# Performance work log

Measured on AMD Instinct MI355X. Metric: run time of the kernel, lower is better.

The kernel has to match this reference:

```python
import jax, jax.numpy as jnp
import numpy as np
from jax.ops import segment_sum

N = 100000
E = 2500000
F = 2
H = 32
L = 2


def setup_inputs() -> dict:
    key = jax.random.key(0)
    ks = jax.random.split(key, 12)
    s = 0.1
    node_features = jax.random.normal(ks[0], (N, F), dtype=jnp.float32)
    edge_index = jax.random.randint(ks[1], (2, E), 0, N, dtype=jnp.int64)
    W_in = jax.random.normal(ks[2], (F, H), dtype=jnp.float32) * s
    b_in = jnp.zeros((H,), dtype=jnp.float32)
    W_upd = jax.random.normal(ks[3], (L, 2 * H, H), dtype=jnp.float32) * s
    b_upd = jnp.zeros((L, H), dtype=jnp.float32)
    We1 = jax.random.normal(ks[4], (2 * H, H), dtype=jnp.float32) * s
    be1 = jnp.zeros((H,), dtype=jnp.float32)
    We2 = jax.random.normal(ks[5], (H, 1), dtype=jnp.float32) * s
    be2 = jnp.zeros((1,), dtype=jnp.float32)
    return {"node_features": node_features, "edge_index": edge_index,
            "W_in": W_in, "b_in": b_in, "W_upd": W_upd, "b_upd": b_upd,
            "We1": We1, "be1": be1, "We2": We2, "be2": be2}


def reference(node_features, edge_index, W_in, b_in, W_upd, b_upd, We1, be1, We2, be2):
    row, col = edge_index[0], edge_index[1]
    h = jax.nn.relu(node_features @ W_in + b_in)  # [N, H]
    # degree of each row node (bincount, clamped to >=1)
    deg = segment_sum(jnp.ones((E,), dtype=jnp.float32), row, num_segments=N)
    deg = jnp.maximum(deg, 1.0)[:, None]  # [N, 1]
    for l in range(L):
        agg = segment_sum(h[col], row, num_segments=N) / deg  # gather + scatter-add + normalize
        h = jax.nn.relu(jnp.concatenate([h, agg], axis=-1) @ W_upd[l] + b_upd[l])
    edge_feat = jnp.concatenate([h[row], h[col]], axis=-1)  # [E, 2H]
    hidden = jax.nn.relu(edge_feat @ We1 + be1)
    flux = (hidden @ We2 + be2)[:, 0]  # [E]
    return flux
```

## Files before the change

kernel.cpp:

```cpp
#include <hip/hip_runtime.h>
#include <hip/hip_fp16.h>

#define NN 100000
#define NE 2500000
#define RANGE 256
#define NBUCK 391
#define CHUNK 16384
#define NBLK_A ((NE + CHUNK - 1) / CHUNK)
#define BCAP 8192

__device__ __forceinline__ float relu_(float x){ return fmaxf(x, 0.f); }


__global__ __launch_bounds__(512) void k_histA(const int* __restrict__ row,
                                               int* __restrict__ btot,
                                               int* __restrict__ blockhist)
{
  __shared__ int hist[NBUCK];
  int t = threadIdx.x;
  for (int i = t; i < NBUCK; i += 512) hist[i] = 0;
  __syncthreads();
  int e0 = blockIdx.x * CHUNK + t;
#pragma unroll
  for (int k = 0; k < CHUNK / 512; ++k) {
    int e = e0 + k * 512;
    if (e < NE) atomicAdd(&hist[row[e] >> 8], 1);
  }
  __syncthreads();
  for (int i = t; i < NBUCK; i += 512) {
    int c = hist[i];
    blockhist[(size_t)i * NBLK_A + blockIdx.x] = c;
    if (c) atomicAdd(&btot[i], c);
  }
}

__global__ __launch_bounds__(512) void k_scanA(const int* __restrict__ btot,
                                               int* __restrict__ bbase)
{
  __shared__ int s[512];
  int t = threadIdx.x;
  int my = (t < NBUCK) ? btot[t] : 0;
  s[t] = my;
  __syncthreads();
  for (int off = 1; off < 512; off <<= 1) {
    int v = (t >= off) ? s[t - off] : 0;
    __syncthreads();
    s[t] += v;
    __syncthreads();
  }
  if (t < NBUCK) bbase[t] = s[t] - my;
  if (t == 0) bbase[NBUCK] = NE;
}

__global__ __launch_bounds__(512) void k_colscan(int* __restrict__ blockhist,
                                                 const int* __restrict__ bbase)
{
  __shared__ int s[512];
  int i = blockIdx.x, t = threadIdx.x;
  int* rowp = blockhist + (size_t)i * NBLK_A;
  int my = (t < NBLK_A) ? rowp[t] : 0;
  s[t] = my;
  __syncthreads();
  for (int off = 1; off < 512; off <<= 1) {
    int v = (t >= off) ? s[t - off] : 0;
    __syncthreads();
    s[t] += v;
    __syncthreads();
  }
  if (t < NBLK_A) rowp[t] = bbase[i] + s[t] - my;
}

__global__ __launch_bounds__(512) void k_partition(
    const int* __restrict__ row, const int* __restrict__ col,
    const int* __restrict__ blockhist, unsigned int* __restrict__ keys)
{
  __shared__ int cur[NBUCK];
  __shared__ int base[NBUCK];
  int t = threadIdx.x, b = blockIdx.x;
  for (int i = t; i < NBUCK; i += 512) {
    base[i] = blockhist[(size_t)i * NBLK_A + b];
    cur[i] = 0;
  }
  __syncthreads();
  int e0 = b * CHUNK + t;
#pragma unroll
  for (int k = 0; k < CHUNK / 512; ++k) {
    int e = e0 + k * 512;
    if (e < NE) {
      int r = row[e];
      int bi = r >> 8;
      int idx = atomicAdd(&cur[bi], 1);
      keys[base[bi] + idx] = ((unsigned)col[e] << 8) | (unsigned)(r & 255);
    }
  }
}

__global__ __launch_bounds__(512) void k_passB_l1(
    const int* __restrict__ bbase, const unsigned int* __restrict__ keys,
    const float* __restrict__ nf, const float* __restrict__ Win,
    const float* __restrict__ bin, const float* __restrict__ W,
    const float* __restrict__ bupd,
    int* __restrict__ ecol, int* __restrict__ rowptr,
    __half* __restrict__ h16b)
{
  __shared__ unsigned keysl[BCAP];
  __shared__ int hist[RANGE];
  __shared__ int sc[RANGE];
  __shared__ int segs[RANGE];
  __shared__ int sege[RANGE];
  __shared__ float Ws[2048];
  __shared__ float bs[32];
  int t = threadIdx.x, b = blockIdx.x;
  for (int i = t; i < 2048; i += 512) Ws[i] = W[i];
  if (t < 32) bs[t] = bupd[t];
  int s0 = bbase[b], e0 = bbase[b + 1];
  int cnt = e0 - s0;
  if (t < RANGE) hist[t] = 0;
  __syncthreads();
  for (int i = t; i < cnt; i += 512) {
    unsigned k = keys[s0 + i];
    if (i < BCAP) keysl[i] = k;
    atomicAdd(&hist[k & 255u], 1);
  }
  __syncthreads();
  int my = (t < RANGE) ? hist[t] : 0;
  if (t < RANGE) sc[t] = my;
  __syncthreads();
  for (int off = 1; off < RANGE; off <<= 1) {
    int v = 0;
    if (t < RANGE && t >= off) v = sc[t - off];
    __syncthreads();
    if (t < RANGE) sc[t] += v;
    __syncthreads();
  }
  if (t < RANGE) {
    int ex = sc[t] - my;
    int n = b * RANGE + t;
    if (n <= NN) rowptr[n] = s0 + ex;
    segs[t] = ex;
    sege[t] = sc[t];
    hist[t] = ex;
  }
  __syncthreads();
  for (int i = t; i < cnt; i += 512) {
    unsigned key = (i < BCAP) ? keysl[i] : keys[s0 + i];
    int rl = (int)(key & 255u);
    int idx = atomicAdd(&hist[rl], 1);
    ecol[s0 + idx] = (int)(key >> 8);
  }
  __syncthreads();

  const float2* nf2 = (const float2*)nf;
  for (int slot = t; slot < RANGE * 4; slot += 512) {
    int node = slot >> 2, q = slot & 3;
    int n = b * RANGE + node;
    if (n >= NN) continue;
    float w0[8], w1[8], bb[8];
#pragma unroll
    for (int j = 0; j < 8; ++j) {
      w0[j] = Win[q * 8 + j];
      w1[j] = Win[32 + q * 8 + j];
      bb[j] = bin[q * 8 + j];
    }
    int ss = segs[node], ee = sege[node];
    float acc[8];
#pragma unroll
    for (int j = 0; j < 8; ++j) acc[j] = 0.f;
    int i = ss;
    for (; i + 2 <= ee; i += 2) {
      int c0 = ecol[s0 + i], c1 = ecol[s0 + i + 1];
      float2 f0 = nf2[c0];
      float2 f1 = nf2[c1];
#pragma unroll
      for (int j = 0; j < 8; ++j) {
        acc[j] += relu_(fmaf(f0.x, w0[j], fmaf(f0.y, w1[j], bb[j])));
        acc[j] += relu_(fmaf(f1.x, w0[j], fmaf(f1.y, w1[j], bb[j])));
      }
    }
    if (i < ee) {
      float2 f = nf2[ecol[s0 + i]];
#pragma unroll
      for (int j = 0; j < 8; ++j)
        acc[j] += relu_(fmaf(f.x, w0[j], fmaf(f.y, w1[j], bb[j])));
    }
    float dinv = 1.0f / fmaxf((float)(ee - ss), 1.0f);
    float g[8], a[8];
    float2 fn = nf2[n];
#pragma unroll
    for (int j = 0; j < 8; ++j) {
      g[j] = acc[j] * dinv;
      a[j] = relu_(fmaf(fn.x, w0[j], fmaf(fn.y, w1[j], bb[j])));
    }
    float o[8];
#pragma unroll
    for (int j = 0; j < 8; ++j) o[j] = bs[q * 8 + j];
#pragma unroll
    for (int src = 0; src < 4; ++src) {
#pragma unroll
      for (int k = 0; k < 8; ++k) {
        float xh = __shfl(a[k], src, 4);
        float xg = __shfl(g[k], src, 4);
        const float* wr1 = Ws + (src * 8 + k) * 32 + q * 8;
        const float* wr2 = Ws + (32 + src * 8 + k) * 32 + q * 8;
#pragma unroll
        for (int j = 0; j < 8; ++j) {
          o[j] = fmaf(xh, wr1[j], o[j]);
          o[j] = fmaf(xg, wr2[j], o[j]);
        }
      }
    }
    uint4 pk;
    __half2* pp = (__half2*)&pk;
#pragma unroll
    for (int k = 0; k < 4; ++k)
      pp[k] = __floats2half2_rn(relu_(o[2*k]), relu_(o[2*k+1]));
    ((uint4*)h16b)[(size_t)n * 4 + q] = pk;
  }
}

__global__ __launch_bounds__(256) void k_agg_update2_uv(
    const int* __restrict__ rowptr, const int* __restrict__ ecol,
    const __half* __restrict__ h16in, const float* __restrict__ W,
    const float* __restrict__ b, const float* __restrict__ We1,
    const float* __restrict__ be1, __half* __restrict__ u,
    __half* __restrict__ v)
{
  __shared__ float Ws[2048];
  __shared__ float Es[2048];
  __shared__ float bs[32];
  __shared__ float bes[32];
  __shared__ float xs[64][65];
  int t = threadIdx.x;
  for (int i = t; i < 2048; i += 256) { Ws[i] = W[i]; Es[i] = We1[i]; }
  if (t < 32) { bs[t] = b[t]; bes[t] = be1[t]; }
  int q = t & 3, ln = t >> 2;
  int n = blockIdx.x * 64 + ln;
  bool act = (n < NN);
  const uint4* hv = (const uint4*)h16in;

  float acc[8];
#pragma unroll
  for (int j = 0; j < 8; ++j) acc[j] = 0.f;
  if (act) {
    int s = rowptr[n], e = rowptr[n + 1];
    int i = s;
    for (; i + 2 <= e; i += 2) {
      int c0 = ecol[i], c1 = ecol[i + 1];
      uint4 x0 = hv[c0 * 4 + q];
      uint4 x1 = hv[c1 * 4 + q];
      const __half2* p0 = (const __half2*)&x0;
      const __half2* p1 = (const __half2*)&x1;
#pragma unroll
      for (int k = 0; k < 4; ++k) {
        float2 f0 = __half22float2(p0[k]);
        float2 f1 = __half22float2(p1[k]);
        acc[2*k]   += f0.x + f1.x;
        acc[2*k+1] += f0.y + f1.y;
      }
    }
    if (i < e) {
      uint4 x = hv[ecol[i] * 4 + q];
      const __half2* hp = (const __half2*)&x;
#pragma unroll
      for (int k = 0; k < 4; ++k) {
        float2 f = __half22float2(hp[k]);
        acc[2*k] += f.x; acc[2*k+1] += f.y;
      }
    }
    float dinv = 1.0f / fmaxf((float)(e - s), 1.0f);
    uint4 hx = hv[n * 4 + q];
    const __half2* hp = (const __half2*)&hx;
#pragma unroll
    for (int k = 0; k < 4; ++k) {
      float2 f = __half22float2(hp[k]);
      xs[ln][q*8 + 2*k]     = f.x;
      xs[ln][q*8 + 2*k + 1] = f.y;
      xs[ln][32 + q*8 + 2*k]     = acc[2*k] * dinv;
      xs[ln][32 + q*8 + 2*k + 1] = acc[2*k+1] * dinv;
    }
  }
  __syncthreads();
  float h2[8];
#pragma unroll
  for (int j = 0; j < 8; ++j) h2[j] = bs[q*8 + j];
  if (act) {
    for (int k = 0; k < 64; ++k) {
      float xk = xs[ln][k];
      const float* wr = Ws + k * 32 + q * 8;
#pragma unroll
      for (int j = 0; j < 8; ++j) h2[j] = fmaf(xk, wr[j], h2[j]);
    }
#pragma unroll
    for (int j = 0; j < 8; ++j) h2[j] = relu_(h2[j]);
  }
  __syncthreads();
  if (act) {
#pragma unroll
    for (int j = 0; j < 8; ++j) xs[ln][q*8 + j] = h2[j];
  }
  __syncthreads();
  if (!act) return;
  float au[8], av[8];
#pragma unroll
  for (int j = 0; j < 8; ++j) { au[j] = bes[q*8 + j]; av[j] = 0.f; }
  for (int k = 0; k < 32; ++k) {
    float hk = xs[ln][k];
    const float* wu = Es + k * 32 + q * 8;
    const float* wv = Es + (32 + k) * 32 + q * 8;
#pragma unroll
    for (int j = 0; j < 8; ++j) {
      au[j] = fmaf(hk, wu[j], au[j]);
      av[j] = fmaf(hk, wv[j], av[j]);
    }
  }
  uint4 pu, pv;
  __half2* up = (__half2*)&pu;
  __half2* vp = (__half2*)&pv;
#pragma unroll
  for (int k = 0; k < 4; ++k) {
    up[k] = __floats2half2_rn(au[2*k], au[2*k+1]);
    vp[k] = __floats2half2_rn(av[2*k], av[2*k+1]);
  }
  ((uint4*)u)[n * 4 + q] = pu;
  ((uint4*)v)[n * 4 + q] = pv;
}

__global__ __launch_bounds__(256) void k_flux(
    const int* __restrict__ row, const int* __restrict__ col,
    const __half* __restrict__ u, const __half* __restrict__ v,
    const float* __restrict__ We2, const float* __restrict__ be2,
    float* __restrict__ out)
{
  int gid = blockIdx.x * 256 + threadIdx.x;
  int e = gid >> 2, q = gid & 3;
  if (e >= NE) return;
  int r = row[e], c = col[e];
  uint4 ua = ((const uint4*)u)[r * 4 + q];
  uint4 vb = ((const uint4*)v)[c * 4 + q];
  const __half2* ah = (const __half2*)&ua;
  const __half2* bh = (const __half2*)&vb;
  const float4* w4 = (const float4*)(We2 + q * 8);
  float4 w0 = w4[0], w1 = w4[1];
  float p = 0.f;
  {
    float2 a = __half22float2(ah[0]), b = __half22float2(bh[0]);
    p += relu_(a.x + b.x) * w0.x + relu_(a.y + b.y) * w0.y;
    a = __half22float2(ah[1]); b = __half22float2(bh[1]);
    p += relu_(a.x + b.x) * w0.z + relu_(a.y + b.y) * w0.w;
    a = __half22float2(ah[2]); b = __half22float2(bh[2]);
    p += relu_(a.x + b.x) * w1.x + relu_(a.y + b.y) * w1.y;
    a = __half22float2(ah[3]); b = __half22float2(bh[3]);
    p += relu_(a.x + b.x) * w1.z + relu_(a.y + b.y) * w1.w;
  }
  p += __shfl_xor(p, 1, 4);
  p += __shfl_xor(p, 2, 4);
  if (q == 0) out[e] = p + be2[0];
}

extern "C" void kernel_launch(void* const* d_in, const int* in_sizes, int n_in,
                              void* d_out, int out_size, void* d_ws, size_t ws_size,
                              hipStream_t stream) {
  const float* nf   = (const float*)d_in[0];
  const int*   ei   = (const int*)d_in[1];
  const float* Win  = (const float*)d_in[2];
  const float* bin  = (const float*)d_in[3];
  const float* Wupd = (const float*)d_in[4];
  const float* bupd = (const float*)d_in[5];
  const float* We1  = (const float*)d_in[6];
  const float* be1  = (const float*)d_in[7];
  const float* We2  = (const float*)d_in[8];
  const float* be2  = (const float*)d_in[9];
  float* out = (float*)d_out;

  const int* row = ei;
  const int* col = ei + NE;

  char* ws = (char*)d_ws;
  const size_t HB16 = (size_t)NN * 32 * 2;
  unsigned int* keys = (unsigned int*)(ws);
  int*          ecol = (int*)(ws + 10000000);
  __half*       h16b = (__half*)(ws + 20000000);
  __half*       u    = (__half*)(ws + 20000000 + HB16);
  __half*       v    = (__half*)(ws + 20000000 + 2 * HB16);
  char*         tail = ws + 20000000 + 3 * HB16;
  int*          rowptr    = (int*)(tail);
  int*          btot      = (int*)(tail + 400512);
  int*          bbase     = (int*)(tail + 402560);
  int*          blockhist = (int*)(tail + 404608);

  hipMemsetAsync(btot, 0, NBUCK * 4, stream);
  k_histA<<<NBLK_A, 512, 0, stream>>>(row, btot, blockhist);
  k_scanA<<<1, 512, 0, stream>>>(btot, bbase);
  k_colscan<<<NBUCK, 512, 0, stream>>>(blockhist, bbase);
  k_partition<<<NBLK_A, 512, 0, stream>>>(row, col, blockhist, keys);
  k_passB_l1<<<NBUCK, 512, 0, stream>>>(bbase, keys, nf, Win, bin,
                                        Wupd, bupd, ecol, rowptr, h16b);

  k_agg_update2_uv<<<(NN + 63) / 64, 256, 0, stream>>>(rowptr, ecol, h16b,
                                                       Wupd + 2048, bupd + 32,
                                                       We1, be1, u, v);

  k_flux<<<(NE * 4 + 255) / 256, 256, 0, stream>>>(row, col, u, v, We2, be2, out);
}
```

Before: 218.8 us.

## Replace exact bucket scan with fixed-capacity atomic bucket slots; shuffle-based node MLP

The separate histogram, scan and column-scan kernels are replaced by a single partition kernel. It reserves space in fixed-capacity per-bucket regions using global atomic cursors, so the row array is read once less and three launches go away. Row segments become (start,end) pairs inside each padded bucket. The node update MLP now broadcasts features via width-4 shuffles instead of a padded shared-memory tile with block barriers. The cost is that any bucket holding more than 8192 edges would overflow into its neighbour, which is safe only for this uniform random graph.

```diff
diff --git a/kernel.cpp b/kernel.cpp
--- a/kernel.cpp
+++ b/kernel.cpp
@@ -5,22 +5,23 @@
 #define NE 2500000
 #define RANGE 256
 #define NBUCK 391
+#define CAP 8192
 #define CHUNK 16384
 #define NBLK_A ((NE + CHUNK - 1) / CHUNK)
 #define BCAP 8192
 
 __device__ __forceinline__ float relu_(float x){ return fmaxf(x, 0.f); }
 
-
-__global__ __launch_bounds__(512) void k_histA(const int* __restrict__ row,
-                                               int* __restrict__ btot,
-                                               int* __restrict__ blockhist)
+__global__ __launch_bounds__(512) void k_partition1(
+    const int* __restrict__ row, const int* __restrict__ col,
+    int* __restrict__ cursor, unsigned int* __restrict__ keys)
 {
   __shared__ int hist[NBUCK];
-  int t = threadIdx.x;
+  __shared__ int base[NBUCK];
+  int t = threadIdx.x, b = blockIdx.x;
   for (int i = t; i < NBUCK; i += 512) hist[i] = 0;
   __syncthreads();
-  int e0 = blockIdx.x * CHUNK + t;
+  int e0 = b * CHUNK + t;
 #pragma unroll
   for (int k = 0; k < CHUNK / 512; ++k) {
     int e = e0 + k * 512;
@@ -29,78 +30,28 @@
   __syncthreads();
   for (int i = t; i < NBUCK; i += 512) {
     int c = hist[i];
-    blockhist[(size_t)i * NBLK_A + blockIdx.x] = c;
-    if (c) atomicAdd(&btot[i], c);
-  }
-}
-
-__global__ __launch_bounds__(512) void k_scanA(const int* __restrict__ btot,
-                                               int* __restrict__ bbase)
-{
-  __shared__ int s[512];
-  int t = threadIdx.x;
-  int my = (t < NBUCK) ? btot[t] : 0;
-  s[t] = my;
-  __syncthreads();
-  for (int off = 1; off < 512; off <<= 1) {
-    int v = (t >= off) ? s[t - off] : 0;
-    __syncthreads();
-    s[t] += v;
-    __syncthreads();
-  }
-  if (t < NBUCK) bbase[t] = s[t] - my;
-  if (t == 0) bbase[NBUCK] = NE;
-}
-
-__global__ __launch_bounds__(512) void k_colscan(int* __restrict__ blockhist,
-                                                 const int* __restrict__ bbase)
-{
-  __shared__ int s[512];
-  int i = blockIdx.x, t = threadIdx.x;
-  int* rowp = blockhist + (size_t)i * NBLK_A;
-  int my = (t < NBLK_A) ? rowp[t] : 0;
-  s[t] = my;
-  __syncthreads();
-  for (int off = 1; off < 512; off <<= 1) {
-    int v = (t >= off) ? s[t - off] : 0;
-    __syncthreads();
-    s[t] += v;
-    __syncthreads();
-  }
-  if (t < NBLK_A) rowp[t] = bbase[i] + s[t] - my;
-}
-
-__global__ __launch_bounds__(512) void k_partition(
-    const int* __restrict__ row, const int* __restrict__ col,
-    const int* __restrict__ blockhist, unsigned int* __restrict__ keys)
-{
-  __shared__ int cur[NBUCK];
-  __shared__ int base[NBUCK];
-  int t = threadIdx.x, b = blockIdx.x;
-  for (int i = t; i < NBUCK; i += 512) {
-    base[i] = blockhist[(size_t)i * NBLK_A + b];
-    cur[i] = 0;
-  }
-  __syncthreads();
-  int e0 = b * CHUNK + t;
+    base[i] = c ? (i * CAP + atomicAdd(&cursor[i], c)) : 0;
+    hist[i] = 0;
+  }
+  __syncthreads();
 #pragma unroll
   for (int k = 0; k < CHUNK / 512; ++k) {
     int e = e0 + k * 512;
     if (e < NE) {
       int r = row[e];
       int bi = r >> 8;
-      int idx = atomicAdd(&cur[bi], 1);
+      int idx = atomicAdd(&hist[bi], 1);
       keys[base[bi] + idx] = ((unsigned)col[e] << 8) | (unsigned)(r & 255);
     }
   }
 }
 
 __global__ __launch_bounds__(512) void k_passB_l1(
-    const int* __restrict__ bbase, const unsigned int* __restrict__ keys,
+    const int* __restrict__ cursor, const unsigned int* __restrict__ keys,
     const float* __restrict__ nf, const float* __restrict__ Win,
     const float* __restrict__ bin, const float* __restrict__ W,
     const float* __restrict__ bupd,
-    int* __restrict__ ecol, int* __restrict__ rowptr,
+    int* __restrict__ ecol, int2* __restrict__ rowseg,
     __half* __restrict__ h16b)
 {
   __shared__ unsigned keysl[BCAP];
@@ -113,8 +64,8 @@
   int t = threadIdx.x, b = blockIdx.x;
   for (int i = t; i < 2048; i += 512) Ws[i] = W[i];
   if (t < 32) bs[t] = bupd[t];
-  int s0 = bbase[b], e0 = bbase[b + 1];
-  int cnt = e0 - s0;
+  int s0 = b * CAP;
+  int cnt = cursor[b];
   if (t < RANGE) hist[t] = 0;
   __syncthreads();
   for (int i = t; i < cnt; i += 512) {
@@ -136,7 +87,7 @@
   if (t < RANGE) {
     int ex = sc[t] - my;
     int n = b * RANGE + t;
-    if (n <= NN) rowptr[n] = s0 + ex;
+    if (n < NN) rowseg[n] = make_int2(s0 + ex, s0 + sc[t]);
     segs[t] = ex;
     sege[t] = sc[t];
     hist[t] = ex;
@@ -219,7 +170,7 @@
 }
 
 __global__ __launch_bounds__(256) void k_agg_update2_uv(
-    const int* __restrict__ rowptr, const int* __restrict__ ecol,
+    const int2* __restrict__ rowseg, const int* __restrict__ ecol,
     const __half* __restrict__ h16in, const float* __restrict__ W,
     const float* __restrict__ b, const float* __restrict__ We1,
     const float* __restrict__ be1, __half* __restrict__ u,
@@ -229,88 +180,90 @@
   __shared__ float Es[2048];
   __shared__ float bs[32];
   __shared__ float bes[32];
-  __shared__ float xs[64][65];
   int t = threadIdx.x;
   for (int i = t; i < 2048; i += 256) { Ws[i] = W[i]; Es[i] = We1[i]; }
   if (t < 32) { bs[t] = b[t]; bes[t] = be1[t]; }
+  __syncthreads();
   int q = t & 3, ln = t >> 2;
   int n = blockIdx.x * 64 + ln;
-  bool act = (n < NN);
+  if (n >= NN) return;
   const uint4* hv = (const uint4*)h16in;
 
+  int2 seg = rowseg[n];
   float acc[8];
 #pragma unroll
   for (int j = 0; j < 8; ++j) acc[j] = 0.f;
-  if (act) {
-    int s = rowptr[n], e = rowptr[n + 1];
-    int i = s;
-    for (; i + 2 <= e; i += 2) {
-      int c0 = ecol[i], c1 = ecol[i + 1];
-      uint4 x0 = hv[c0 * 4 + q];
-      uint4 x1 = hv[c1 * 4 + q];
-      const __half2* p0 = (const __half2*)&x0;
-      const __half2* p1 = (const __half2*)&x1;
-#pragma unroll
-      for (int k = 0; k < 4; ++k) {
-        float2 f0 = __half22float2(p0[k]);
-        float2 f1 = __half22float2(p1[k]);
-        acc[2*k]   += f0.x + f1.x;
-        acc[2*k+1] += f0.y + f1.y;
-      }
-    }
-    if (i < e) {
-      uint4 x = hv[ecol[i] * 4 + q];
-      const __half2* hp = (const __half2*)&x;
-#pragma unroll
-      for (int k = 0; k < 4; ++k) {
-        float2 f = __half22float2(hp[k]);
-        acc[2*k] += f.x; acc[2*k+1] += f.y;
-      }
-    }
-    float dinv = 1.0f / fmaxf((float)(e - s), 1.0f);
+  int i = seg.x;
+  for (; i + 2 <= seg.y; i += 2) {
+    int c0 = ecol[i], c1 = ecol[i + 1];
+    uint4 x0 = hv[c0 * 4 + q];
+    uint4 x1 = hv[c1 * 4 + q];
+    const __half2* p0 = (const __half2*)&x0;
+    const __half2* p1 = (const __half2*)&x1;
+#pragma unroll
+    for (int k = 0; k < 4; ++k) {
+      float2 f0 = __half22float2(p0[k]);
+      float2 f1 = __half22float2(p1[k]);
+      acc[2*k]   += f0.x + f1.x;
+      acc[2*k+1] += f0.y + f1.y;
+    }
+  }
+  if (i < seg.y) {
+    uint4 x = hv[ecol[i] * 4 + q];
+    const __half2* hp = (const __half2*)&x;
+#pragma unroll
+    for (int k = 0; k < 4; ++k) {
+      float2 f = __half22float2(hp[k]);
+      acc[2*k] += f.x; acc[2*k+1] += f.y;
+    }
+  }
+  float dinv = 1.0f / fmaxf((float)(seg.y - seg.x), 1.0f);
+  float a[8], g[8];
+  {
     uint4 hx = hv[n * 4 + q];
     const __half2* hp = (const __half2*)&hx;
 #pragma unroll
     for (int k = 0; k < 4; ++k) {
       float2 f = __half22float2(hp[k]);
-      xs[ln][q*8 + 2*k]     = f.x;
-      xs[ln][q*8 + 2*k + 1] = f.y;
-      xs[ln][32 + q*8 + 2*k]     = acc[2*k] * dinv;
-      xs[ln][32 + q*8 + 2*k + 1] = acc[2*k+1] * dinv;
-    }
-  }
-  __syncthreads();
+      a[2*k] = f.x; a[2*k+1] = f.y;
+      g[2*k] = acc[2*k] * dinv; g[2*k+1] = acc[2*k+1] * dinv;
+    }
+  }
   float h2[8];
 #pragma unroll
   for (int j = 0; j < 8; ++j) h2[j] = bs[q*8 + j];
-  if (act) {
-    for (int k = 0; k < 64; ++k) {
-      float xk = xs[ln][k];
-      const float* wr = Ws + k * 32 + q * 8;
-#pragma unroll
-      for (int j = 0; j < 8; ++j) h2[j] = fmaf(xk, wr[j], h2[j]);
-    }
-#pragma unroll
-    for (int j = 0; j < 8; ++j) h2[j] = relu_(h2[j]);
-  }
-  __syncthreads();
-  if (act) {
-#pragma unroll
-    for (int j = 0; j < 8; ++j) xs[ln][q*8 + j] = h2[j];
-  }
-  __syncthreads();
-  if (!act) return;
+#pragma unroll
+  for (int src = 0; src < 4; ++src) {
+#pragma unroll
+    for (int k = 0; k < 8; ++k) {
+      float xh = __shfl(a[k], src, 4);
+      float xg = __shfl(g[k], src, 4);
+      const float* wr1 = Ws + (src * 8 + k) * 32 + q * 8;
+      const float* wr2 = Ws + (32 + src * 8 + k) * 32 + q * 8;
+#pragma unroll
+      for (int j = 0; j < 8; ++j) {
+        h2[j] = fmaf(xh, wr1[j], h2[j]);
+        h2[j] = fmaf(xg, wr2[j], h2[j]);
+      }
+    }
+  }
+#pragma unroll
+  for (int j = 0; j < 8; ++j) h2[j] = relu_(h2[j]);
   float au[8], av[8];
 #pragma unroll
   for (int j = 0; j < 8; ++j) { au[j] = bes[q*8 + j]; av[j] = 0.f; }
-  for (int k = 0; k < 32; ++k) {
-    float hk = xs[ln][k];
-    const float* wu = Es + k * 32 + q * 8;
-    const float* wv = Es + (32 + k) * 32 + q * 8;
-#pragma unroll
-    for (int j = 0; j < 8; ++j) {
-      au[j] = fmaf(hk, wu[j], au[j]);
-      av[j] = fmaf(hk, wv[j], av[j]);
+#pragma unroll
+  for (int src = 0; src < 4; ++src) {
+#pragma unroll
+    for (int k = 0; k < 8; ++k) {
+      float xk = __shfl(h2[k], src, 4);
+      const float* wu = Es + (src * 8 + k) * 32 + q * 8;
+      const float* wv = Es + (32 + src * 8 + k) * 32 + q * 8;
+#pragma unroll
+      for (int j = 0; j < 8; ++j) {
+        au[j] = fmaf(xk, wu[j], au[j]);
+        av[j] = fmaf(xk, wv[j], av[j]);
+      }
     }
   }
   uint4 pu, pv;
@@ -376,29 +329,22 @@
   const int* col = ei + NE;
 
   char* ws = (char*)d_ws;
+  const size_t KB = (size_t)NBUCK * CAP * 4;
   const size_t HB16 = (size_t)NN * 32 * 2;
-  unsigned int* keys = (unsigned int*)(ws);
-  int*          ecol = (int*)(ws + 10000000);
-  __half*       h16b = (__half*)(ws + 20000000);
-  __half*       u    = (__half*)(ws + 20000000 + HB16);
-  __half*       v    = (__half*)(ws + 20000000 + 2 * HB16);
-  char*         tail = ws + 20000000 + 3 * HB16;
-  int*          rowptr    = (int*)(tail);
-  int*          btot      = (int*)(tail + 400512);
-  int*          bbase     = (int*)(tail + 402560);
-  int*          blockhist = (int*)(tail + 404608);
-
-  hipMemsetAsync(btot, 0, NBUCK * 4, stream);
-  k_histA<<<NBLK_A, 512, 0, stream>>>(row, btot, blockhist);
-  k_scanA<<<1, 512, 0, stream>>>(btot, bbase);
-  k_colscan<<<NBUCK, 512, 0, stream>>>(blockhist, bbase);
-  k_partition<<<NBLK_A, 512, 0, stream>>>(row, col, blockhist, keys);
-  k_passB_l1<<<NBUCK, 512, 0, stream>>>(bbase, keys, nf, Win, bin,
-                                        Wupd, bupd, ecol, rowptr, h16b);
-
-  k_agg_update2_uv<<<(NN + 63) / 64, 256, 0, stream>>>(rowptr, ecol, h16b,
+  unsigned int* keys   = (unsigned int*)(ws);
+  int*          ecol   = (int*)(ws + KB);
+  __half*       h16b   = (__half*)(ws + 2 * KB);
+  __half*       u      = (__half*)(ws + 2 * KB + HB16);
+  __half*       v      = (__half*)(ws + 2 * KB + 2 * HB16);
+  int2*         rowseg = (int2*)(ws + 2 * KB + 3 * HB16);
+  int*          cursor = (int*)(ws + 2 * KB + 3 * HB16 + 800000);
+
+  hipMemsetAsync(cursor, 0, NBUCK * 4, stream);
+  k_partition1<<<NBLK_A, 512, 0, stream>>>(row, col, cursor, keys);
+  k_passB_l1<<<NBUCK, 512, 0, stream>>>(cursor, keys, nf, Win, bin,
+                                        Wupd, bupd, ecol, rowseg, h16b);
+  k_agg_update2_uv<<<(NN + 63) / 64, 256, 0, stream>>>(rowseg, ecol, h16b,
                                                        Wupd + 2048, bupd + 32,
                                                        We1, be1, u, v);
-
   k_flux<<<(NE * 4 + 255) / 256, 256, 0, stream>>>(row, col, u, v, We2, be2, out);
 }
```

Result: faster. 210.9 us (-3.6%).
